# Kernel tuning notes

Measured on AMD Instinct MI355X. Metric: run time of the kernel, lower is better.

Reference implementation:

```python
import jax, jax.numpy as jnp
import numpy as np

DIM = 128
EXPAND = 2
INTERNAL = DIM * EXPAND  # 256
MAX_SEQ = 2048
BATCH = 32
GATE_DECAY = 3.0


def _gated_cell(x, Wa, ba, Wi, bi, g):
    # x: [B,S,D]; Wa,Wi: [E,D]; ba,bi,g: [E]
    pa = jnp.einsum('bsd,ed->bse', x, Wa) + ba          # projected activation
    pi = jnp.einsum('bsd,ed->bse', x, Wi) + bi          # projected input
    reset_gate = jax.nn.sigmoid(pa)
    input_gate = jax.nn.sigmoid(pi)
    alpha = jax.nn.sigmoid(g)                           # [E]
    a = alpha / jnp.power(GATE_DECAY, reset_gate)       # adaptive alpha [B,S,E]
    u = jnp.sqrt(1.0 - a * a) * (input_gate * pi)       # per-step input [B,S,E]

    def step(h, au):
        a_t, u_t = au
        h = a_t * h + u_t
        return h, h

    h0 = jnp.zeros((x.shape[0], Wa.shape[0]), x.dtype)
    _, ys = jax.lax.scan(step, h0, (a.transpose(1, 0, 2), u.transpose(1, 0, 2)))
    return ys.transpose(1, 0, 2)                        # [B,S,E]


def _recency_weights(seq_len, dtype):
    w = jnp.exp(jnp.linspace(0.0, 3.0, MAX_SEQ))[:seq_len]
    return w.astype(dtype).reshape(1, -1, 1)


def setup_inputs() -> dict:
    key = jax.random.key(0)
    ks = jax.random.split(key, 12)
    std = 1.0 / np.sqrt(DIM)  # kaiming fan_in linear
    lo = float(np.log(0.9 / 0.1))
    hi = float(np.log(0.999 / 0.001))
    d = {
        'x': jax.random.normal(ks[0], (BATCH, MAX_SEQ, DIM), jnp.float32),
        'Wa_u': jax.random.normal(ks[1], (INTERNAL, DIM), jnp.float32) * std,
        'ba_u': jnp.zeros((INTERNAL,), jnp.float32),
        'Wi_u': jax.random.normal(ks[2], (INTERNAL, DIM), jnp.float32) * std,
        'bi_u': jnp.zeros((INTERNAL,), jnp.float32),
        'g_u': jax.random.uniform(ks[3], (INTERNAL,), jnp.float32, lo, hi),
        'Wa_w': jax.random.normal(ks[4], (INTERNAL, DIM), jnp.float32) * std,
        'ba_w': jnp.zeros((INTERNAL,), jnp.float32),
        'Wi_w': jax.random.normal(ks[5], (INTERNAL, DIM), jnp.float32) * std,
        'bi_w': jnp.zeros((INTERNAL,), jnp.float32),
        'g_w': jax.random.uniform(ks[6], (INTERNAL,), jnp.float32, lo, hi),
        'Wf': jax.random.normal(ks[7], (DIM, 4 * DIM), jnp.float32) * (1.0 / np.sqrt(4 * DIM)),
        'bf': jnp.zeros((DIM,), jnp.float32),
    }
    return d


def reference(x, Wa_u, ba_u, Wi_u, bi_u, g_u, Wa_w, ba_w, Wi_w, bi_w, g_w, Wf, bf):
    unweighted = _gated_cell(x, Wa_u, ba_u, Wi_u, bi_u, g_u)          # [B,S,2D]
    xw = x * _recency_weights(x.shape[1], x.dtype)
    weighted = _gated_cell(xw, Wa_w, ba_w, Wi_w, bi_w, g_w)           # [B,S,2D]
    combined = jnp.concatenate([unweighted, weighted], axis=-1)       # [B,S,4D]
    return jnp.einsum('bsf,df->bsd', combined, Wf) + bf               # [B,S,D]
```

## Files before the change

### kernel.cpp

```cpp
#include <hip/hip_runtime.h>
#include <hip/hip_fp16.h>
#include <cstddef>
#include <cstdint>

#define DIM 128
#define SEQ 2048
#define NB 32
#define NCH 512
#define NROWS (NB * SEQ)

typedef _Float16 half8 __attribute__((ext_vector_type(8)));
typedef float    f32x4 __attribute__((ext_vector_type(4)));

#define CMB_BYTES ((size_t)NROWS * NCH * 2)
#define WFG_OFF   CMB_BYTES
#define WFG_BYTES ((size_t)NCH * DIM * 2)
#define XH_OFF    (WFG_OFF + WFG_BYTES)
#define XH_BYTES  ((size_t)NROWS * DIM * 2)
#define WS_NEEDED (XH_OFF + XH_BYTES)

__device__ __forceinline__ float sigf(float v) {
    return 1.0f / (1.0f + __expf(-v));
}

__global__ void k0_prep(const float* __restrict__ x, const float* __restrict__ Wf,
                        _Float16* __restrict__ xh, _Float16* __restrict__ Wfg) {
    int bid = blockIdx.x;
    if (bid < 4096) {
        int g = bid * 256 + threadIdx.x;
        const float* src = x + (size_t)g * 8;
        float4 v0 = *(const float4*)src;
        float4 v1 = *(const float4*)(src + 4);
        half8 hv;
        hv[0] = (_Float16)v0.x; hv[1] = (_Float16)v0.y;
        hv[2] = (_Float16)v0.z; hv[3] = (_Float16)v0.w;
        hv[4] = (_Float16)v1.x; hv[5] = (_Float16)v1.y;
        hv[6] = (_Float16)v1.z; hv[7] = (_Float16)v1.w;
        *(half8*)(xh + (size_t)g * 8) = hv;
    } else {
        int t = (bid - 4096) * 256 + threadIdx.x;
#pragma unroll
        for (int i = 0; i < 8; ++i) {
            int o = t * 8 + i;
            int j    = o & 7;
            int lane = (o >> 3) & 63;
            int q    = lane >> 4, n16 = lane & 15;
            int ct   = (o >> 9) & 7;
            int ks   = (o >> 12) & 1;
            int kb   = o >> 13;
            int k = kb * 64 + ks * 32 + q * 8 + j;
            int n = ct * 16 + n16;
            Wfg[o] = (_Float16)Wf[n * NCH + k];
        }
    }
}

__global__ __launch_bounds__(256, 4) void kfused(
        const _Float16* __restrict__ xh,
        const float* __restrict__ Wa_u, const float* __restrict__ ba_u,
        const float* __restrict__ Wi_u, const float* __restrict__ bi_u,
        const float* __restrict__ g_u,
        const float* __restrict__ Wa_w, const float* __restrict__ ba_w,
        const float* __restrict__ Wi_w, const float* __restrict__ bi_w,
        const float* __restrict__ g_w,
        _Float16* __restrict__ cmb) {
    __shared__ _Float16 Bs[4096];
    __shared__ float2   seg[16][17];
    __shared__ float    pref[16][17];
    __shared__ float    carry[16];

    const int tid  = threadIdx.x;
    const int lane = tid & 63;
    const int w    = tid >> 6;
    const int quad = lane >> 4;
    const int n16  = lane & 15;

    const int b  = blockIdx.x;
    const int cg = blockIdx.y;
    const int p  = cg >> 4;
    const int ebase = (cg & 15) * 16;

    const float* Wa  = p ? Wa_w : Wa_u;
    const float* Wi  = p ? Wi_w : Wi_u;
    const float* bap = p ? ba_w : ba_u;
    const float* bip = p ? bi_w : bi_u;
    const float* gp  = p ? g_w  : g_u;

    for (int sl = tid; sl < 512; sl += 256) {
        int l  = sl & 63;
        int nt = (sl >> 6) & 1;
        int ks = sl >> 7;
        int qq = l >> 4, nn = l & 15;
        int e = ebase + nn;
        const float* Wp = nt ? Wi : Wa;
        const float* src = Wp + (size_t)e * DIM + ks * 32 + qq * 8;
        float4 v0 = *(const float4*)src;
        float4 v1 = *(const float4*)(src + 4);
        half8 hv;
        hv[0] = (_Float16)v0.x; hv[1] = (_Float16)v0.y;
        hv[2] = (_Float16)v0.z; hv[3] = (_Float16)v0.w;
        hv[4] = (_Float16)v1.x; hv[5] = (_Float16)v1.y;
        hv[6] = (_Float16)v1.z; hv[7] = (_Float16)v1.w;
        *(half8*)&Bs[sl * 8] = hv;
    }

    const int e = ebase + n16;
    const float rba = bap[e];
    const float rbi = bip[e];
    const float ral = sigf(gp[e]);
    if (tid < 16) carry[tid] = 0.0f;

    float scb = __expf((float)(w * 16 + quad * 4) * (3.0f / 2047.0f));
    const float r1   = __expf(3.0f / 2047.0f);
    const float r2   = r1 * r1;
    const float r3   = r2 * r1;
    const float cs64 = __expf(64.0f * 3.0f / 2047.0f);

    const _Float16* xrow = xh + (size_t)b * SEQ * DIM;
    _Float16* cmbb = cmb + (size_t)b * SEQ * NCH + cg * 16 + n16;

    __syncthreads();

    half8 af[4];
    {
        const _Float16* ab = xrow + (size_t)(w * 16 + n16) * DIM + quad * 8;
#pragma unroll
        for (int ks = 0; ks < 4; ++ks) af[ks] = *(const half8*)(ab + ks * 32);
    }

    for (int t = 0; t < 32; ++t) {
        const int s0 = t * 64;

        f32x4 acc[2];
        acc[0] = (f32x4){0.f, 0.f, 0.f, 0.f};
        acc[1] = (f32x4){0.f, 0.f, 0.f, 0.f};
#pragma unroll
        for (int ks = 0; ks < 4; ++ks) {
            half8 a = af[ks];
            half8 b0 = *(const half8*)&Bs[(ks * 128 + lane) * 8];
            half8 b1 = *(const half8*)&Bs[(ks * 128 + 64 + lane) * 8];
            acc[0] = __builtin_amdgcn_mfma_f32_16x16x32_f16(a, b0, acc[0], 0, 0, 0);
            acc[1] = __builtin_amdgcn_mfma_f32_16x16x32_f16(a, b1, acc[1], 0, 0, 0);
        }

        {
            int tn = (t + 1) & 31;
            const _Float16* ab = xrow + (size_t)(tn * 64 + w * 16 + n16) * DIM + quad * 8;
#pragma unroll
            for (int ks = 0; ks < 4; ++ks) af[ks] = *(const half8*)(ab + ks * 32);
        }

        float sc[4];
        if (p) { sc[0] = scb; sc[1] = scb * r1; sc[2] = scb * r2; sc[3] = scb * r3; }
        else   { sc[0] = sc[1] = sc[2] = sc[3] = 1.0f; }
        scb *= cs64;

        float a_s[4], u_s[4];
        float A4 = 1.0f, U4 = 0.0f;
#pragma unroll
        for (int reg = 0; reg < 4; ++reg) {
            float pa = fmaf(acc[0][reg], sc[reg], rba);
            float pi = fmaf(acc[1][reg], sc[reg], rbi);
            float rst = sigf(pa);
            float ig  = sigf(pi);
            float a   = ral * exp2f(-rst * 1.5849625007211562f);
            float u   = sqrtf(fmaxf(1.0f - a * a, 0.0f)) * ig * pi;
            a_s[reg] = a; u_s[reg] = u;
            A4 *= a;
            U4 = fmaf(a, U4, u);
        }
        seg[w * 4 + quad][n16] = make_float2(A4, U4);
        __syncthreads();

        if (tid < 16) {
            float H = carry[tid];
#pragma unroll
            for (int ts = 0; ts < 16; ++ts) {
                float2 AU = seg[ts][tid];
                pref[ts][tid] = H;
                H = fmaf(AU.x, H, AU.y);
            }
            carry[tid] = H;
        }
        __syncthreads();

        {
            float h = pref[w * 4 + quad][n16];
            _Float16* dst = cmbb + (size_t)(s0 + w * 16 + quad * 4) * NCH;
#pragma unroll
            for (int reg = 0; reg < 4; ++reg) {
                h = fmaf(a_s[reg], h, u_s[reg]);
                dst[(size_t)reg * NCH] = (_Float16)h;
            }
        }
    }
}

__global__ __launch_bounds__(256, 4) void k3_mfma(
        const _Float16* __restrict__ cmb, const _Float16* __restrict__ Wfg,
        const float* __restrict__ bfv, float* __restrict__ out) {
    __shared__ _Float16 As[8 * 512];
    __shared__ _Float16 Bs[16 * 512];

    const int tid  = threadIdx.x;
    const int lane = tid & 63;
    const int w    = tid >> 6;
    const int row0 = blockIdx.x * 64;
    const int q    = lane >> 4;
    const int nn   = lane & 15;

    f32x4 acc[8];
#pragma unroll
    for (int ct = 0; ct < 8; ++ct) acc[ct] = (f32x4){0.0f, 0.0f, 0.0f, 0.0f};

    for (int kb = 0; kb < 8; ++kb) {
        const int kc = kb * 64;
#pragma unroll
        for (int i = 0; i < 2; ++i) {
            int f = tid + i * 256;
            int r = f >> 3, k8 = f & 7;
            uint4 v = *(const uint4*)(cmb + (size_t)(row0 + r) * NCH + kc + k8 * 8);
            int mt = r >> 4, m = r & 15, ks = k8 >> 2, qq = k8 & 3;
            *(uint4*)&As[(((mt * 2 + ks) * 64) + qq * 16 + m) * 8] = v;
        }
#pragma unroll
        for (int i = 0; i < 4; ++i) {
            int f = tid + i * 256;
            uint4 v = *(const uint4*)(Wfg + (size_t)kb * 8192 + (size_t)f * 8);
            *(uint4*)&Bs[(size_t)f * 8] = v;
        }
        __syncthreads();

#pragma unroll
        for (int ks = 0; ks < 2; ++ks) {
            half8 a0 = *(const half8*)&As[((w * 2 + ks) * 64 + lane) * 8];
#pragma unroll
            for (int ct = 0; ct < 8; ++ct) {
                half8 bb = *(const half8*)&Bs[((ks * 8 + ct) * 64 + lane) * 8];
                acc[ct] = __builtin_amdgcn_mfma_f32_16x16x32_f16(a0, bb, acc[ct], 0, 0, 0);
            }
        }
        __syncthreads();
    }

    int rbase = row0 + w * 16 + q * 4;
#pragma unroll
    for (int ct = 0; ct < 8; ++ct) {
        int col = ct * 16 + nn;
        float bias = bfv[col];
#pragma unroll
        for (int reg = 0; reg < 4; ++reg)
            out[(size_t)(rbase + reg) * DIM + col] = acc[ct][reg] + bias;
    }
}

extern "C" void kernel_launch(void* const* d_in, const int* in_sizes, int n_in,
                              void* d_out, int out_size, void* d_ws, size_t ws_size,
                              hipStream_t stream) {
    if (ws_size < WS_NEEDED) return;

    const float* x    = (const float*)d_in[0];
    const float* Wa_u = (const float*)d_in[1];
    const float* ba_u = (const float*)d_in[2];
    const float* Wi_u = (const float*)d_in[3];
    const float* bi_u = (const float*)d_in[4];
    const float* g_u  = (const float*)d_in[5];
    const float* Wa_w = (const float*)d_in[6];
    const float* ba_w = (const float*)d_in[7];
    const float* Wi_w = (const float*)d_in[8];
    const float* bi_w = (const float*)d_in[9];
    const float* g_w  = (const float*)d_in[10];
    const float* Wf   = (const float*)d_in[11];
    const float* bfv  = (const float*)d_in[12];
    float* out = (float*)d_out;

    char* ws = (char*)d_ws;
    _Float16* cmb = (_Float16*)ws;
    _Float16* Wfg = (_Float16*)(ws + WFG_OFF);
    _Float16* xh  = (_Float16*)(ws + XH_OFF);

    hipLaunchKernelGGL(k0_prep, dim3(4128), dim3(256), 0, stream, x, Wf, xh, Wfg);
    hipLaunchKernelGGL(kfused, dim3(32, 32), dim3(256), 0, stream,
                       xh, Wa_u, ba_u, Wi_u, bi_u, g_u,
                       Wa_w, ba_w, Wi_w, bi_w, g_w, cmb);
    hipLaunchKernelGGL(k3_mfma, dim3(1024), dim3(256), 0, stream,
                       cmb, Wfg, bfv, out);
}
```

Before: 203.5 us.

## Drop fp16 x prep pass and enlarge final GEMM row tile

```diff
diff --git a/kernel.cpp b/kernel.cpp
--- a/kernel.cpp
+++ b/kernel.cpp
@@ -15,48 +15,31 @@
 #define CMB_BYTES ((size_t)NROWS * NCH * 2)
 #define WFG_OFF   CMB_BYTES
 #define WFG_BYTES ((size_t)NCH * DIM * 2)
-#define XH_OFF    (WFG_OFF + WFG_BYTES)
-#define XH_BYTES  ((size_t)NROWS * DIM * 2)
-#define WS_NEEDED (XH_OFF + XH_BYTES)
+#define WS_NEEDED (WFG_OFF + WFG_BYTES)
 
 __device__ __forceinline__ float sigf(float v) {
     return 1.0f / (1.0f + __expf(-v));
 }
 
-__global__ void k0_prep(const float* __restrict__ x, const float* __restrict__ Wf,
-                        _Float16* __restrict__ xh, _Float16* __restrict__ Wfg) {
-    int bid = blockIdx.x;
-    if (bid < 4096) {
-        int g = bid * 256 + threadIdx.x;
-        const float* src = x + (size_t)g * 8;
-        float4 v0 = *(const float4*)src;
-        float4 v1 = *(const float4*)(src + 4);
-        half8 hv;
-        hv[0] = (_Float16)v0.x; hv[1] = (_Float16)v0.y;
-        hv[2] = (_Float16)v0.z; hv[3] = (_Float16)v0.w;
-        hv[4] = (_Float16)v1.x; hv[5] = (_Float16)v1.y;
-        hv[6] = (_Float16)v1.z; hv[7] = (_Float16)v1.w;
-        *(half8*)(xh + (size_t)g * 8) = hv;
-    } else {
-        int t = (bid - 4096) * 256 + threadIdx.x;
-#pragma unroll
-        for (int i = 0; i < 8; ++i) {
-            int o = t * 8 + i;
-            int j    = o & 7;
-            int lane = (o >> 3) & 63;
-            int q    = lane >> 4, n16 = lane & 15;
-            int ct   = (o >> 9) & 7;
-            int ks   = (o >> 12) & 1;
-            int kb   = o >> 13;
-            int k = kb * 64 + ks * 32 + q * 8 + j;
-            int n = ct * 16 + n16;
-            Wfg[o] = (_Float16)Wf[n * NCH + k];
-        }
+__global__ void k0_wfg(const float* __restrict__ Wf, _Float16* __restrict__ Wfg) {
+    int t = blockIdx.x * 256 + threadIdx.x;
+#pragma unroll
+    for (int i = 0; i < 8; ++i) {
+        int o = t * 8 + i;
+        int j    = o & 7;
+        int lane = (o >> 3) & 63;
+        int q    = lane >> 4, n16 = lane & 15;
+        int ct   = (o >> 9) & 7;
+        int ks   = (o >> 12) & 1;
+        int kb   = o >> 13;
+        int k = kb * 64 + ks * 32 + q * 8 + j;
+        int n = ct * 16 + n16;
+        Wfg[o] = (_Float16)Wf[n * NCH + k];
     }
 }
 
 __global__ __launch_bounds__(256, 4) void kfused(
-        const _Float16* __restrict__ xh,
+        const float* __restrict__ x,
         const float* __restrict__ Wa_u, const float* __restrict__ ba_u,
         const float* __restrict__ Wi_u, const float* __restrict__ bi_u,
         const float* __restrict__ g_u,
@@ -116,20 +99,32 @@
     const float r3   = r2 * r1;
     const float cs64 = __expf(64.0f * 3.0f / 2047.0f);
 
-    const _Float16* xrow = xh + (size_t)b * SEQ * DIM;
+    const float* xbase = x + ((size_t)b * SEQ + (size_t)(w * 16 + n16)) * DIM + quad * 8;
     _Float16* cmbb = cmb + (size_t)b * SEQ * NCH + cg * 16 + n16;
 
     __syncthreads();
 
-    half8 af[4];
-    {
-        const _Float16* ab = xrow + (size_t)(w * 16 + n16) * DIM + quad * 8;
-#pragma unroll
-        for (int ks = 0; ks < 4; ++ks) af[ks] = *(const half8*)(ab + ks * 32);
+    float4 xf[8];
+#pragma unroll
+    for (int ks = 0; ks < 4; ++ks) {
+        xf[2 * ks]     = *(const float4*)(xbase + ks * 32);
+        xf[2 * ks + 1] = *(const float4*)(xbase + ks * 32 + 4);
     }
 
     for (int t = 0; t < 32; ++t) {
         const int s0 = t * 64;
+
+        half8 af[4];
+#pragma unroll
+        for (int ks = 0; ks < 4; ++ks) {
+            float4 v0 = xf[2 * ks], v1 = xf[2 * ks + 1];
+            half8 hv;
+            hv[0] = (_Float16)v0.x; hv[1] = (_Float16)v0.y;
+            hv[2] = (_Float16)v0.z; hv[3] = (_Float16)v0.w;
+            hv[4] = (_Float16)v1.x; hv[5] = (_Float16)v1.y;
+            hv[6] = (_Float16)v1.z; hv[7] = (_Float16)v1.w;
+            af[ks] = hv;
+        }
 
         f32x4 acc[2];
         acc[0] = (f32x4){0.f, 0.f, 0.f, 0.f};
@@ -145,9 +140,12 @@
 
         {
             int tn = (t + 1) & 31;
-            const _Float16* ab = xrow + (size_t)(tn * 64 + w * 16 + n16) * DIM + quad * 8;
-#pragma unroll
-            for (int ks = 0; ks < 4; ++ks) af[ks] = *(const half8*)(ab + ks * 32);
+            const float* ab = xbase + (size_t)tn * 64 * DIM;
+#pragma unroll
+            for (int ks = 0; ks < 4; ++ks) {
+                xf[2 * ks]     = *(const float4*)(ab + ks * 32);
+                xf[2 * ks + 1] = *(const float4*)(ab + ks * 32 + 4);
+            }
         }
 
         float sc[4];
@@ -196,32 +194,35 @@
     }
 }
 
-__global__ __launch_bounds__(256, 4) void k3_mfma(
+__global__ __launch_bounds__(256, 2) void k3_mfma(
         const _Float16* __restrict__ cmb, const _Float16* __restrict__ Wfg,
         const float* __restrict__ bfv, float* __restrict__ out) {
-    __shared__ _Float16 As[8 * 512];
+    __shared__ _Float16 As[16 * 512];
     __shared__ _Float16 Bs[16 * 512];
 
     const int tid  = threadIdx.x;
     const int lane = tid & 63;
     const int w    = tid >> 6;
-    const int row0 = blockIdx.x * 64;
+    const int row0 = blockIdx.x * 128;
     const int q    = lane >> 4;
     const int nn   = lane & 15;
 
-    f32x4 acc[8];
-#pragma unroll
-    for (int ct = 0; ct < 8; ++ct) acc[ct] = (f32x4){0.0f, 0.0f, 0.0f, 0.0f};
+    f32x4 acc[2][8];
+#pragma unroll
+    for (int rt = 0; rt < 2; ++rt)
+#pragma unroll
+        for (int ct = 0; ct < 8; ++ct)
+            acc[rt][ct] = (f32x4){0.0f, 0.0f, 0.0f, 0.0f};
 
     for (int kb = 0; kb < 8; ++kb) {
         const int kc = kb * 64;
 #pragma unroll
-        for (int i = 0; i < 2; ++i) {
+        for (int i = 0; i < 4; ++i) {
             int f = tid + i * 256;
             int r = f >> 3, k8 = f & 7;
             uint4 v = *(const uint4*)(cmb + (size_t)(row0 + r) * NCH + kc + k8 * 8);
-            int mt = r >> 4, m = r & 15, ks = k8 >> 2, qq = k8 & 3;
-            *(uint4*)&As[(((mt * 2 + ks) * 64) + qq * 16 + m) * 8] = v;
+            int rt = r >> 4, m = r & 15, ks = k8 >> 2, qq = k8 & 3;
+            *(uint4*)&As[(((rt * 2 + ks) * 64) + qq * 16 + m) * 8] = v;
         }
 #pragma unroll
         for (int i = 0; i < 4; ++i) {
@@ -233,24 +234,29 @@
 
 #pragma unroll
         for (int ks = 0; ks < 2; ++ks) {
-            half8 a0 = *(const half8*)&As[((w * 2 + ks) * 64 + lane) * 8];
+            half8 a0 = *(const half8*)&As[(((w * 2 + 0) * 2 + ks) * 512) + lane * 8];
+            half8 a1 = *(const half8*)&As[(((w * 2 + 1) * 2 + ks) * 512) + lane * 8];
 #pragma unroll
             for (int ct = 0; ct < 8; ++ct) {
-                half8 bb = *(const half8*)&Bs[((ks * 8 + ct) * 64 + lane) * 8];
-                acc[ct] = __builtin_amdgcn_mfma_f32_16x16x32_f16(a0, bb, acc[ct], 0, 0, 0);
-            }
-        }
-        __syncthreads();
-    }
-
-    int rbase = row0 + w * 16 + q * 4;
-#pragma unroll
-    for (int ct = 0; ct < 8; ++ct) {
-        int col = ct * 16 + nn;
-        float bias = bfv[col];
-#pragma unroll
-        for (int reg = 0; reg < 4; ++reg)
-            out[(size_t)(rbase + reg) * DIM + col] = acc[ct][reg] + bias;
+                half8 bb = *(const half8*)&Bs[((ks * 8 + ct) * 512) + lane * 8];
+                acc[0][ct] = __builtin_amdgcn_mfma_f32_16x16x32_f16(a0, bb, acc[0][ct], 0, 0, 0);
+                acc[1][ct] = __builtin_amdgcn_mfma_f32_16x16x32_f16(a1, bb, acc[1][ct], 0, 0, 0);
+            }
+        }
+        __syncthreads();
+    }
+
+#pragma unroll
+    for (int rt = 0; rt < 2; ++rt) {
+        int rbase = row0 + w * 32 + rt * 16 + q * 4;
+#pragma unroll
+        for (int ct = 0; ct < 8; ++ct) {
+            int col = ct * 16 + nn;
+            float bias = bfv[col];
+#pragma unroll
+            for (int reg = 0; reg < 4; ++reg)
+                out[(size_t)(rbase + reg) * DIM + col] = acc[rt][ct][reg] + bias;
+        }
     }
 }
 
@@ -277,12 +283,11 @@
     char* ws = (char*)d_ws;
     _Float16* cmb = (_Float16*)ws;
     _Float16* Wfg = (_Float16*)(ws + WFG_OFF);
-    _Float16* xh  = (_Float16*)(ws + XH_OFF);
-
-    hipLaunchKernelGGL(k0_prep, dim3(4128), dim3(256), 0, stream, x, Wf, xh, Wfg);
+
+    hipLaunchKernelGGL(k0_wfg, dim3(32), dim3(256), 0, stream, Wf, Wfg);
     hipLaunchKernelGGL(kfused, dim3(32, 32), dim3(256), 0, stream,
-                       xh, Wa_u, ba_u, Wi_u, bi_u, g_u,
+                       x, Wa_u, ba_u, Wi_u, bi_u, g_u,
                        Wa_w, ba_w, Wi_w, bi_w, g_w, cmb);
-    hipLaunchKernelGGL(k3_mfma, dim3(1024), dim3(256), 0, stream,
+    hipLaunchKernelGGL(k3_mfma, dim3(512), dim3(256), 0, stream,
                        cmb, Wfg, bfv, out);
 }
```

Measured after the change: 241.8 us. 1.19x slower.
